# Optimization experiments

Hardware: AMD Instinct MI355X
Metric: run time of the kernel (lower is better)

Reference implementation:

```python
import jax, jax.numpy as jnp
import numpy as np

TEMPERATURE = 100.0  # exponential-smoothing temperature from __init__ default
ETA = 1.0            # feature/label cost tradeoff


def _cdist(a, b):
    # Euclidean distance matrix [M, N] between rows of a [M, D] and b [N, D]
    sq = (jnp.sum(a * a, axis=1)[:, None]
          + jnp.sum(b * b, axis=1)[None, :]
          - 2.0 * (a @ b.T))
    return jnp.sqrt(jnp.maximum(sq, 1e-12))


def setup_inputs() -> dict:
    key = jax.random.key(0)
    ks = jax.random.split(key, 9)
    B, Nt, Ns, H, Wd, C = 1024, 8192, 8192, 32, 32, 10
    D = H * Wd
    x = jax.random.normal(ks[0], (B, H, Wd), jnp.float32)
    target_features = jax.random.normal(ks[1], (Nt, H, Wd), jnp.float32)
    aligned_source_features = jax.random.normal(ks[2], (Nt, H, Wd), jnp.float32)
    source_features = jax.random.normal(ks[3], (Ns, H, Wd), jnp.float32)
    source_high_dim_labels = jax.random.uniform(ks[4], (Ns, C), jnp.float32)
    aligned_target_labels = jax.random.uniform(ks[5], (Ns, C), jnp.float32)
    source_label_distances = jax.random.uniform(ks[6], (C, C), jnp.float32)
    W = jax.random.normal(ks[7], (D, C), jnp.float32) * 0.02
    b = jnp.zeros((C,), jnp.float32)
    return {
        "x": x,
        "target_features": target_features,
        "aligned_source_features": aligned_source_features,
        "source_features": source_features,
        "source_high_dim_labels": source_high_dim_labels,
        "aligned_target_labels": aligned_target_labels,
        "source_label_distances": source_label_distances,
        "W": W,
        "b": b,
    }


def reference(x, target_features, aligned_source_features, source_features,
              source_high_dim_labels, aligned_target_labels,
              source_label_distances, W, b):
    B = x.shape[0]
    xf = x.reshape(B, -1)                                   # [B, D]
    tf = target_features.reshape(target_features.shape[0], -1)       # [Nt, D]
    asf = aligned_source_features.reshape(aligned_source_features.shape[0], -1)  # [Nt, D]
    sf = source_features.reshape(source_features.shape[0], -1)       # [Ns, D]

    # --- feature transport: target -> source (plain_softmax) ---
    d_feat = _cdist(xf, tf)                                 # [B, Nt]
    w_feat = jax.nn.softmax(-TEMPERATURE * d_feat, axis=1)  # [B, Nt]
    x_src = w_feat @ asf                                    # [B, D] in source space

    # --- source model (linear classifier head -> soft predictions) ---
    preds = jax.nn.softmax(x_src @ W + b, axis=1)           # [B, C]

    # --- label transport: source -> target (plain_softmax) ---
    cost = _cdist(x_src, sf)                                # feature_dists=True: [B, Ns]
    # label_dists=True: cost of moving predicted label mass to each sample's label
    cost = cost + ETA * (preds @ source_label_distances @ source_high_dim_labels.T)
    w_lab = jax.nn.softmax(-TEMPERATURE * cost, axis=1)     # [B, Ns]
    y = w_lab @ aligned_target_labels                       # [B, C] in target label space
    return y
```

## Files before the change

### kernel.cpp

```cpp
#include <hip/hip_runtime.h>
#include <hip/hip_bf16.h>
#include <math.h>

#define B_ROWS 1024
#define NT 8192
#define NS 8192
#define DIM 1024
#define NC 10
#define TEMP 100.0f
#define WCAP 1024
#define PREP_RPB 8

typedef __bf16 bf16x8 __attribute__((ext_vector_type(8)));
typedef __bf16 bf16x4 __attribute__((ext_vector_type(4)));
typedef float f32x4 __attribute__((ext_vector_type(4)));

#define GLOAD_LDS(g, l) \
    __builtin_amdgcn_global_load_lds((__attribute__((address_space(1))) void*)(g), \
                                     (__attribute__((address_space(3))) void*)(l), 16, 0, 0)

__device__ inline __bf16 split_hi(float v) { return (__bf16)v; }
__device__ inline __bf16 split_lo(float v) {
    __bf16 h = (__bf16)v;
    return (__bf16)(v - (float)h);
}

__device__ inline float wave_max(float v) {
    #pragma unroll
    for (int off = 32; off > 0; off >>= 1)
        v = fmaxf(v, __shfl_down(v, off, 64));
    return v;
}
__device__ inline float wave_sum(float v) {
    #pragma unroll
    for (int off = 32; off > 0; off >>= 1)
        v += __shfl_down(v, off, 64);
    return v;
}

__global__ __launch_bounds__(256) void k_prep0(const float* __restrict__ x,
                                               const float* __restrict__ tf,
                                               const float* __restrict__ sf,
                                               const float* __restrict__ sld,
                                               const float* __restrict__ shdl,
                                               const float* __restrict__ atl,
                                               __bf16* __restrict__ x2,
                                               __bf16* __restrict__ tf2,
                                               __bf16* __restrict__ sf2,
                                               float* __restrict__ nx_,
                                               float* __restrict__ nt_,
                                               float* __restrict__ ns_,
                                               float* __restrict__ M2Tt,
                                               float* __restrict__ atlt) {
    __shared__ float sred[4][PREP_RPB];
    __shared__ float sldL[NC * NC];
    const int NXB = B_ROWS / PREP_RPB;
    const int NTB = NT / PREP_RPB;
    const int NSB = NS / PREP_RPB;
    int b = blockIdx.x;
    int tid = threadIdx.x;
    if (b < NXB + NTB + NSB) {
        const float* Xp; __bf16* X2p; float* np; int r0;
        if (b < NXB)            { Xp = x;  X2p = x2;  np = nx_; r0 = b * PREP_RPB; }
        else if (b < NXB + NTB) { Xp = tf; X2p = tf2; np = nt_; r0 = (b - NXB) * PREP_RPB; }
        else                    { Xp = sf; X2p = sf2; np = ns_; r0 = (b - NXB - NTB) * PREP_RPB; }
        int c = tid * 4;
        int lane = tid & 63, wid = tid >> 6;
        #pragma unroll
        for (int r = 0; r < PREP_RPB; r++) {
            float4 v = *(const float4*)(Xp + (size_t)(r0 + r) * DIM + c);
            bf16x4 h, l;
            h[0] = split_hi(v.x); l[0] = split_lo(v.x);
            h[1] = split_hi(v.y); l[1] = split_lo(v.y);
            h[2] = split_hi(v.z); l[2] = split_lo(v.z);
            h[3] = split_hi(v.w); l[3] = split_lo(v.w);
            *(bf16x4*)(X2p + (size_t)(r0 + r) * 2048 + c) = h;
            *(bf16x4*)(X2p + (size_t)(r0 + r) * 2048 + 1024 + c) = l;
            float acc = v.x * v.x + v.y * v.y + v.z * v.z + v.w * v.w;
            float w = wave_sum(acc);
            if (lane == 0) sred[wid][r] = w;
        }
        __syncthreads();
        if (tid < PREP_RPB)
            np[r0 + tid] = sred[0][tid] + sred[1][tid] + sred[2][tid] + sred[3][tid];
    } else {
        if (tid < NC * NC) sldL[tid] = sld[tid];
        __syncthreads();
        int j = (b - NXB - NTB - NSB) * 256 + tid;
        float sh[NC], at[NC];
        #pragma unroll
        for (int k = 0; k < NC; k++) sh[k] = shdl[(size_t)j * NC + k];
        #pragma unroll
        for (int c = 0; c < NC; c++) at[c] = atl[(size_t)j * NC + c];
        #pragma unroll
        for (int c = 0; c < NC; c++) {
            float t = 0.f;
            #pragma unroll
            for (int k = 0; k < NC; k++) t += sldL[c * NC + k] * sh[k];
            M2Tt[c * NS + j] = t;
            atlt[c * NS + j] = at[c];
        }
    }
}

template <bool LOGITS>
__global__ __launch_bounds__(256) void k_gemm3(const __bf16* __restrict__ A2,
                                               const __bf16* __restrict__ B2,
                                               float* __restrict__ C,
                                               int M, int N, int K, int ksplit,
                                               const float* __restrict__ rowN,
                                               const float* __restrict__ colN) {
    __shared__ unsigned short AhS[8192], AlS[8192], BhS[8192], BlS[8192];
    __shared__ float extraL[LOGITS ? 256 : 2];
    float* rnL = extraL;
    float* cnL = extraL + 128;

    int tid = threadIdx.x;
    int wid = tid >> 6, lane = tid & 63;
    int wm = (wid >> 1) * 64, wn = (wid & 1) * 64;
    int id = blockIdx.y * gridDim.x + blockIdx.x;
    int bn_i = ((id >> 6) << 3) | (id & 7);
    int bm_i = (id >> 3) & 7;
    int bm = bm_i * 128, bn = bn_i * 128;
    size_t K2 = 2 * (size_t)K;
    int k_begin = blockIdx.z * ksplit;
    int nsteps = ksplit >> 6;

    if (LOGITS) {
        if (tid < 128) rnL[tid] = rowN[bm + tid];
        else cnL[tid - 128] = colN[bn + tid - 128];
    }

    f32x4 acc[4][4];
    #pragma unroll
    for (int i = 0; i < 4; i++)
        #pragma unroll
        for (int j = 0; j < 4; j++) acc[i][j] = (f32x4){0.f, 0.f, 0.f, 0.f};

    int r_in = lane >> 3;
    int cgo = ((lane & 7) ^ r_in) * 8;
    const __bf16* gA = A2 + (size_t)(bm + wid * 32 + r_in) * K2 + k_begin + cgo;
    const __bf16* gB = B2 + (size_t)(bn + wid * 32 + r_in) * K2 + k_begin + cgo;
    char* AhB = (char*)AhS; char* AlB = (char*)AlS;
    char* BhB = (char*)BhS; char* BlB = (char*)BlS;
    int lbw = wid * 4096;
    size_t row8 = 8 * K2;

    int ra = lane & 15, q = lane >> 4;
    int aoff[4][2], boff[4][2];
    #pragma unroll
    for (int i = 0; i < 4; i++) {
        #pragma unroll
        for (int kh = 0; kh < 2; kh++) {
            int chunk = ((kh << 2) | q) ^ (ra & 7);
            aoff[i][kh] = (wm + i * 16 + ra) * 64 + chunk * 8;
            boff[i][kh] = (wn + i * 16 + ra) * 64 + chunk * 8;
        }
    }
    const __bf16* AhE = (const __bf16*)AhS;
    const __bf16* AlE = (const __bf16*)AlS;
    const __bf16* BhE = (const __bf16*)BhS;
    const __bf16* BlE = (const __bf16*)BlS;

    for (int ks = 0; ks < nsteps; ks++) {
        __syncthreads();
        #pragma unroll
        for (int p = 0; p < 4; p++) {
            size_t go = p * row8;
            int lo = lbw + p * 1024;
            GLOAD_LDS(gA + go, AhB + lo);
            GLOAD_LDS(gA + go + K, AlB + lo);
            GLOAD_LDS(gB + go, BhB + lo);
            GLOAD_LDS(gB + go + K, BlB + lo);
        }
        gA += 64; gB += 64;
        __syncthreads();

        #pragma unroll
        for (int kh = 0; kh < 2; kh++) {
            bf16x8 ah[4], al[4];
            #pragma unroll
            for (int mi = 0; mi < 4; mi++) {
                ah[mi] = *(const bf16x8*)(AhE + aoff[mi][kh]);
                al[mi] = *(const bf16x8*)(AlE + aoff[mi][kh]);
            }
            #pragma unroll
            for (int ni = 0; ni < 4; ni++) {
                bf16x8 bh = *(const bf16x8*)(BhE + boff[ni][kh]);
                bf16x8 bl = *(const bf16x8*)(BlE + boff[ni][kh]);
                #pragma unroll
                for (int mi = 0; mi < 4; mi++) {
                    acc[mi][ni] = __builtin_amdgcn_mfma_f32_16x16x32_bf16(ah[mi], bh, acc[mi][ni], 0, 0, 0);
                    acc[mi][ni] = __builtin_amdgcn_mfma_f32_16x16x32_bf16(ah[mi], bl, acc[mi][ni], 0, 0, 0);
                    acc[mi][ni] = __builtin_amdgcn_mfma_f32_16x16x32_bf16(al[mi], bh, acc[mi][ni], 0, 0, 0);
                }
            }
        }
    }

    if (!LOGITS) {
        float* Cb = C + (size_t)blockIdx.z * M * N;
        #pragma unroll
        for (int mi = 0; mi < 4; mi++) {
            #pragma unroll
            for (int ni = 0; ni < 4; ni++) {
                int r0 = bm + wm + mi * 16 + q * 4;
                int c0 = bn + wn + ni * 16 + ra;
                Cb[(size_t)(r0 + 0) * N + c0] = acc[mi][ni][0];
                Cb[(size_t)(r0 + 1) * N + c0] = acc[mi][ni][1];
                Cb[(size_t)(r0 + 2) * N + c0] = acc[mi][ni][2];
                Cb[(size_t)(r0 + 3) * N + c0] = acc[mi][ni][3];
            }
        }
    } else {
        #pragma unroll
        for (int mi = 0; mi < 4; mi++) {
            #pragma unroll
            for (int ni = 0; ni < 4; ni++) {
                int cl = wn + ni * 16 + ra;
                float cn = cnL[cl];
                #pragma unroll
                for (int i = 0; i < 4; i++) {
                    int rl = wm + mi * 16 + q * 4 + i;
                    float sq = rnL[rl] + cn - 2.f * acc[mi][ni][i];
                    float d = sqrtf(fmaxf(sq, 1e-12f));
                    C[(size_t)(bm + rl) * N + bn + cl] = -TEMP * d;
                }
            }
        }
    }
}

__global__ __launch_bounds__(256) void k_xsrc(const float* __restrict__ S,
                                              const float* __restrict__ asf,
                                              const float* __restrict__ W,
                                              const float* __restrict__ bias,
                                              __bf16* __restrict__ xsrc2,
                                              float* __restrict__ nx2_,
                                              float* __restrict__ preds) {
    __shared__ float sm[4];
    __shared__ float ss[4];
    __shared__ int   sidx[WCAP];
    __shared__ float swt[WCAP];
    __shared__ int   scnt;
    __shared__ float red[4][NC + 1];
    int row = blockIdx.x;
    int tid = threadIdx.x;
    int lane = tid & 63, wid = tid >> 6;
    if (tid == 0) scnt = 0;
    const float4* sr = (const float4*)(S + (size_t)row * NT);
    float4 vals[NT / 1024];
    float lmax = -1e30f;
    #pragma unroll
    for (int u = 0; u < NT / 1024; u++) {
        float4 v = sr[tid + u * 256];
        vals[u] = v;
        lmax = fmaxf(fmaxf(fmaxf(v.x, v.y), fmaxf(v.z, v.w)), lmax);
    }
    float wmx = wave_max(lmax);
    if (lane == 0) sm[wid] = wmx;
    __syncthreads();
    float bmax = fmaxf(fmaxf(sm[0], sm[1]), fmaxf(sm[2], sm[3]));
    float lsum = 0.f;
    #pragma unroll
    for (int u = 0; u < NT / 1024; u++) {
        float4 v = vals[u];
        v.x = __expf(v.x - bmax); v.y = __expf(v.y - bmax);
        v.z = __expf(v.z - bmax); v.w = __expf(v.w - bmax);
        vals[u] = v;
        lsum += v.x + v.y + v.z + v.w;
    }
    float wsv = wave_sum(lsum);
    if (lane == 0) ss[wid] = wsv;
    __syncthreads();
    float bsum = ss[0] + ss[1] + ss[2] + ss[3];
    float inv = 1.0f / bsum;
    float thr = 1e-8f * bsum;
    #pragma unroll
    for (int u = 0; u < NT / 1024; u++) {
        float4 v = vals[u];
        int j = (tid + u * 256) * 4;
        if (v.x > thr) { int k = atomicAdd(&scnt, 1); if (k < WCAP) { sidx[k] = j;     swt[k] = v.x * inv; } }
        if (v.y > thr) { int k = atomicAdd(&scnt, 1); if (k < WCAP) { sidx[k] = j + 1; swt[k] = v.y * inv; } }
        if (v.z > thr) { int k = atomicAdd(&scnt, 1); if (k < WCAP) { sidx[k] = j + 2; swt[k] = v.z * inv; } }
        if (v.w > thr) { int k = atomicAdd(&scnt, 1); if (k < WCAP) { sidx[k] = j + 3; swt[k] = v.w * inv; } }
    }
    __syncthreads();
    int cnt = scnt < WCAP ? scnt : WCAP;
    int c = tid * 4;
    float sx = 0.f, sy = 0.f, sz = 0.f, sw = 0.f;
    for (int i = 0; i < cnt; i++) {
        float wg = swt[i];
        float4 v = *(const float4*)(asf + (size_t)sidx[i] * DIM + c);
        sx += wg * v.x; sy += wg * v.y; sz += wg * v.z; sw += wg * v.w;
    }
    bf16x4 h, l;
    h[0] = split_hi(sx); l[0] = split_lo(sx);
    h[1] = split_hi(sy); l[1] = split_lo(sy);
    h[2] = split_hi(sz); l[2] = split_lo(sz);
    h[3] = split_hi(sw); l[3] = split_lo(sw);
    *(bf16x4*)(xsrc2 + (size_t)row * 2048 + c) = h;
    *(bf16x4*)(xsrc2 + (size_t)row * 2048 + 1024 + c) = l;
    float accn = sx * sx + sy * sy + sz * sz + sw * sw;
    float accp[NC];
    #pragma unroll
    for (int cc = 0; cc < NC; cc++)
        accp[cc] = sx * W[(c + 0) * NC + cc] + sy * W[(c + 1) * NC + cc]
                 + sz * W[(c + 2) * NC + cc] + sw * W[(c + 3) * NC + cc];
    accn = wave_sum(accn);
    #pragma unroll
    for (int cc = 0; cc < NC; cc++) accp[cc] = wave_sum(accp[cc]);
    if (lane == 0) {
        red[wid][0] = accn;
        #pragma unroll
        for (int cc = 0; cc < NC; cc++) red[wid][1 + cc] = accp[cc];
    }
    __syncthreads();
    if (tid == 0) {
        nx2_[row] = red[0][0] + red[1][0] + red[2][0] + red[3][0];
        float lo[NC];
        float m = -1e30f;
        #pragma unroll
        for (int cc = 0; cc < NC; cc++) {
            lo[cc] = red[0][1 + cc] + red[1][1 + cc] + red[2][1 + cc] + red[3][1 + cc]
                   + bias[cc];
            m = fmaxf(m, lo[cc]);
        }
        float ssum = 0.f;
        #pragma unroll
        for (int cc = 0; cc < NC; cc++) {
            lo[cc] = __expf(lo[cc] - m);
            ssum += lo[cc];
        }
        float iv = 1.0f / ssum;
        #pragma unroll
        for (int cc = 0; cc < NC; cc++) preds[(size_t)row * NC + cc] = lo[cc] * iv;
    }
}

__global__ __launch_bounds__(256) void k_lab_softmax_y(const float* __restrict__ S,
                                                       const float* __restrict__ predsG,
                                                       const float* __restrict__ M2Tt,
                                                       const float* __restrict__ atlt,
                                                       float* __restrict__ y) {
    int r0 = blockIdx.x * 2, r1 = r0 + 1;
    float pr0[NC], pr1[NC];
    #pragma unroll
    for (int c = 0; c < NC; c++) {
        pr0[c] = TEMP * predsG[(size_t)r0 * NC + c];
        pr1[c] = TEMP * predsG[(size_t)r1 * NC + c];
    }
    const float4* s0 = (const float4*)(S + (size_t)r0 * NS);
    const float4* s1 = (const float4*)(S + (size_t)r1 * NS);
    const float4* M2 = (const float4*)M2Tt;
    const float4* AT = (const float4*)atlt;
    float4 v0[NS / 1024], v1[NS / 1024];
    float m0 = -1e30f, m1 = -1e30f;
    #pragma unroll
    for (int u = 0; u < NS / 1024; u++) {
        int j4 = threadIdx.x + u * 256;
        float4 a = s0[j4], b = s1[j4];
        float4 lab0 = make_float4(0.f, 0.f, 0.f, 0.f);
        float4 lab1 = make_float4(0.f, 0.f, 0.f, 0.f);
        #pragma unroll
        for (int c = 0; c < NC; c++) {
            float4 mv = M2[c * 2048 + j4];
            lab0.x += pr0[c] * mv.x; lab0.y += pr0[c] * mv.y;
            lab0.z += pr0[c] * mv.z; lab0.w += pr0[c] * mv.w;
            lab1.x += pr1[c] * mv.x; lab1.y += pr1[c] * mv.y;
            lab1.z += pr1[c] * mv.z; lab1.w += pr1[c] * mv.w;
        }
        a.x -= lab0.x; a.y -= lab0.y;
        a.z -= lab0.z; a.w -= lab0.w;
        b.x -= lab1.x; b.y -= lab1.y;
        b.z -= lab1.z; b.w -= lab1.w;
        v0[u] = a; v1[u] = b;
        m0 = fmaxf(m0, fmaxf(fmaxf(a.x, a.y), fmaxf(a.z, a.w)));
        m1 = fmaxf(m1, fmaxf(fmaxf(b.x, b.y), fmaxf(b.z, b.w)));
    }
    __shared__ float sm[2][4];
    __shared__ float ss[2][4];
    __shared__ float yred[4][2][NC];
    int lane = threadIdx.x & 63, wid = threadIdx.x >> 6;
    float wm0 = wave_max(m0), wm1 = wave_max(m1);
    if (lane == 0) { sm[0][wid] = wm0; sm[1][wid] = wm1; }
    __syncthreads();
    float bm0 = fmaxf(fmaxf(sm[0][0], sm[0][1]), fmaxf(sm[0][2], sm[0][3]));
    float bm1 = fmaxf(fmaxf(sm[1][0], sm[1][1]), fmaxf(sm[1][2], sm[1][3]));
    float ls0 = 0.f, ls1 = 0.f;
    #pragma unroll
    for (int u = 0; u < NS / 1024; u++) {
        float4 a = v0[u], b = v1[u];
        a.x = __expf(a.x - bm0); a.y = __expf(a.y - bm0);
        a.z = __expf(a.z - bm0); a.w = __expf(a.w - bm0);
        b.x = __expf(b.x - bm1); b.y = __expf(b.y - bm1);
        b.z = __expf(b.z - bm1); b.w = __expf(b.w - bm1);
        v0[u] = a; v1[u] = b;
        ls0 += a.x + a.y + a.z + a.w;
        ls1 += b.x + b.y + b.z + b.w;
    }
    float ws0 = wave_sum(ls0), ws1 = wave_sum(ls1);
    if (lane == 0) { ss[0][wid] = ws0; ss[1][wid] = ws1; }
    __syncthreads();
    float inv0 = 1.0f / (ss[0][0] + ss[0][1] + ss[0][2] + ss[0][3]);
    float inv1 = 1.0f / (ss[1][0] + ss[1][1] + ss[1][2] + ss[1][3]);
    float y0[NC] = {}, y1[NC] = {};
    #pragma unroll
    for (int u = 0; u < NS / 1024; u++) {
        int j4 = threadIdx.x + u * 256;
        float4 a = v0[u], b = v1[u];
        #pragma unroll
        for (int c = 0; c < NC; c++) {
            float4 av = AT[c * 2048 + j4];
            y0[c] += a.x * av.x + a.y * av.y + a.z * av.z + a.w * av.w;
            y1[c] += b.x * av.x + b.y * av.y + b.z * av.z + b.w * av.w;
        }
    }
    #pragma unroll
    for (int c = 0; c < NC; c++) {
        y0[c] = wave_sum(y0[c]) * inv0;
        y1[c] = wave_sum(y1[c]) * inv1;
    }
    if (lane == 0) {
        #pragma unroll
        for (int c = 0; c < NC; c++) { yred[wid][0][c] = y0[c]; yred[wid][1][c] = y1[c]; }
    }
    __syncthreads();
    if (threadIdx.x < 2 * NC) {
        int r = threadIdx.x / NC, c = threadIdx.x - r * NC;
        y[(size_t)(r0 + r) * NC + c] = yred[0][r][c] + yred[1][r][c] + yred[2][r][c] + yred[3][r][c];
    }
}

extern "C" void kernel_launch(void* const* d_in, const int* in_sizes, int n_in,
                              void* d_out, int out_size, void* d_ws, size_t ws_size,
                              hipStream_t stream) {
    const float* x    = (const float*)d_in[0];
    const float* tf   = (const float*)d_in[1];
    const float* asf  = (const float*)d_in[2];
    const float* sf   = (const float*)d_in[3];
    const float* shdl = (const float*)d_in[4];
    const float* atl  = (const float*)d_in[5];
    const float* sld  = (const float*)d_in[6];
    const float* W    = (const float*)d_in[7];
    const float* bias = (const float*)d_in[8];
    float* y = (float*)d_out;

    char* wsb = (char*)d_ws;
    float*  S     = (float*)(wsb);
    __bf16* tf2   = (__bf16*)(wsb + (32u << 20));
    __bf16* sf2   = (__bf16*)(wsb + (64u << 20));
    __bf16* x2    = (__bf16*)(wsb + (96u << 20));
    __bf16* xsrc2 = (__bf16*)(wsb + (100u << 20));
    float*  nt_   = (float*)(wsb + (108u << 20));
    float*  ns_   = nt_ + NT;
    float*  nx_   = ns_ + NS;
    float*  nx2_  = nx_ + B_ROWS;
    float*  preds = nx2_ + B_ROWS;
    float*  M2Tt  = preds + B_ROWS * NC;
    float*  atlt  = M2Tt + NS * NC;

    {
        int nblk = B_ROWS / PREP_RPB + NT / PREP_RPB + NS / PREP_RPB + NS / 256;
        k_prep0<<<nblk, 256, 0, stream>>>(x, tf, sf, sld, shdl, atl,
                                          x2, tf2, sf2, nx_, nt_, ns_, M2Tt, atlt);
    }

    {
        dim3 g(NT / 128, B_ROWS / 128, 1);
        k_gemm3<true><<<g, 256, 0, stream>>>(x2, tf2, S, B_ROWS, NT, DIM, DIM,
                                             nx_, nt_);
    }

    k_xsrc<<<B_ROWS, 256, 0, stream>>>(S, asf, W, bias, xsrc2, nx2_, preds);

    {
        dim3 g(NS / 128, B_ROWS / 128, 1);
        k_gemm3<true><<<g, 256, 0, stream>>>(xsrc2, sf2, S, B_ROWS, NS, DIM, DIM,
                                             nx2_, ns_);
    }
    k_lab_softmax_y<<<B_ROWS / 2, 256, 0, stream>>>(S, preds, M2Tt, atlt, y);
}
```

Before: 269.6 us.

## Double-buffer LDS tiles in split-bf16 GEMM with per-wave array loading

```diff
diff --git a/kernel.cpp b/kernel.cpp
--- a/kernel.cpp
+++ b/kernel.cpp
@@ -110,7 +110,8 @@
                                                int M, int N, int K, int ksplit,
                                                const float* __restrict__ rowN,
                                                const float* __restrict__ colN) {
-    __shared__ unsigned short AhS[8192], AlS[8192], BhS[8192], BlS[8192];
+    __shared__ __align__(16) unsigned short AhS[2][4096], AlS[2][4096];
+    __shared__ __align__(16) unsigned short BhS[2][4096], BlS[2][4096];
     __shared__ float extraL[LOGITS ? 256 : 2];
     float* rnL = extraL;
     float* cnL = extraL + 128;
@@ -124,7 +125,7 @@
     int bm = bm_i * 128, bn = bn_i * 128;
     size_t K2 = 2 * (size_t)K;
     int k_begin = blockIdx.z * ksplit;
-    int nsteps = ksplit >> 6;
+    int nsteps = ksplit >> 5;
 
     if (LOGITS) {
         if (tid < 128) rnL[tid] = rowN[bm + tid];
@@ -137,66 +138,66 @@
         #pragma unroll
         for (int j = 0; j < 4; j++) acc[i][j] = (f32x4){0.f, 0.f, 0.f, 0.f};
 
-    int r_in = lane >> 3;
-    int cgo = ((lane & 7) ^ r_in) * 8;
-    const __bf16* gA = A2 + (size_t)(bm + wid * 32 + r_in) * K2 + k_begin + cgo;
-    const __bf16* gB = B2 + (size_t)(bn + wid * 32 + r_in) * K2 + k_begin + cgo;
-    char* AhB = (char*)AhS; char* AlB = (char*)AlS;
-    char* BhB = (char*)BhS; char* BlB = (char*)BlS;
-    int lbw = wid * 4096;
-    size_t row8 = 8 * K2;
+    char* arrB = (wid == 0) ? (char*)AhS : (wid == 1) ? (char*)AlS
+               : (wid == 2) ? (char*)BhS : (char*)BlS;
+    const __bf16* gbase = (wid < 2) ? A2 : B2;
+    int rbase = (wid < 2) ? bm : bn;
+    int hilo = (wid & 1) ? K : 0;
+    int srow = lane >> 2;
+    int kperm = 8 * ((lane & 3) ^ ((lane >> 3) & 3));
+    const __bf16* gw = gbase + (size_t)(rbase + srow) * K2 + hilo + k_begin + kperm;
+    size_t row16 = 16 * K2;
 
     int ra = lane & 15, q = lane >> 4;
-    int aoff[4][2], boff[4][2];
+    int slot = q ^ ((ra >> 1) & 3);
+    int aoff[4], boff[4];
     #pragma unroll
     for (int i = 0; i < 4; i++) {
-        #pragma unroll
-        for (int kh = 0; kh < 2; kh++) {
-            int chunk = ((kh << 2) | q) ^ (ra & 7);
-            aoff[i][kh] = (wm + i * 16 + ra) * 64 + chunk * 8;
-            boff[i][kh] = (wn + i * 16 + ra) * 64 + chunk * 8;
-        }
-    }
-    const __bf16* AhE = (const __bf16*)AhS;
-    const __bf16* AlE = (const __bf16*)AlS;
-    const __bf16* BhE = (const __bf16*)BhS;
-    const __bf16* BlE = (const __bf16*)BlS;
-
+        aoff[i] = (wm + i * 16 + ra) * 32 + slot * 8;
+        boff[i] = (wn + i * 16 + ra) * 32 + slot * 8;
+    }
+
+#define STAGE(buf, koff) do {                                                  \
+        const __bf16* _g = gw + (koff);                                        \
+        char* _d = arrB + (buf) * 8192;                                        \
+        _Pragma("unroll")                                                      \
+        for (int p = 0; p < 8; p++)                                            \
+            GLOAD_LDS(_g + (size_t)p * row16, _d + p * 1024);                  \
+    } while (0)
+
+    STAGE(0, 0);
+    __syncthreads();
+
+    int cur = 0;
     for (int ks = 0; ks < nsteps; ks++) {
-        __syncthreads();
-        #pragma unroll
-        for (int p = 0; p < 4; p++) {
-            size_t go = p * row8;
-            int lo = lbw + p * 1024;
-            GLOAD_LDS(gA + go, AhB + lo);
-            GLOAD_LDS(gA + go + K, AlB + lo);
-            GLOAD_LDS(gB + go, BhB + lo);
-            GLOAD_LDS(gB + go + K, BlB + lo);
-        }
-        gA += 64; gB += 64;
-        __syncthreads();
-
-        #pragma unroll
-        for (int kh = 0; kh < 2; kh++) {
-            bf16x8 ah[4], al[4];
+        if (ks + 1 < nsteps) STAGE(cur ^ 1, (ks + 1) * 32);
+
+        const __bf16* AhE = (const __bf16*)&AhS[cur][0];
+        const __bf16* AlE = (const __bf16*)&AlS[cur][0];
+        const __bf16* BhE = (const __bf16*)&BhS[cur][0];
+        const __bf16* BlE = (const __bf16*)&BlS[cur][0];
+
+        bf16x8 ah[4], al[4];
+        #pragma unroll
+        for (int mi = 0; mi < 4; mi++) {
+            ah[mi] = *(const bf16x8*)(AhE + aoff[mi]);
+            al[mi] = *(const bf16x8*)(AlE + aoff[mi]);
+        }
+        #pragma unroll
+        for (int ni = 0; ni < 4; ni++) {
+            bf16x8 bh = *(const bf16x8*)(BhE + boff[ni]);
+            bf16x8 bl = *(const bf16x8*)(BlE + boff[ni]);
             #pragma unroll
             for (int mi = 0; mi < 4; mi++) {
-                ah[mi] = *(const bf16x8*)(AhE + aoff[mi][kh]);
-                al[mi] = *(const bf16x8*)(AlE + aoff[mi][kh]);
+                acc[mi][ni] = __builtin_amdgcn_mfma_f32_16x16x32_bf16(ah[mi], bh, acc[mi][ni], 0, 0, 0);
+                acc[mi][ni] = __builtin_amdgcn_mfma_f32_16x16x32_bf16(ah[mi], bl, acc[mi][ni], 0, 0, 0);
+                acc[mi][ni] = __builtin_amdgcn_mfma_f32_16x16x32_bf16(al[mi], bh, acc[mi][ni], 0, 0, 0);
             }
-            #pragma unroll
-            for (int ni = 0; ni < 4; ni++) {
-                bf16x8 bh = *(const bf16x8*)(BhE + boff[ni][kh]);
-                bf16x8 bl = *(const bf16x8*)(BlE + boff[ni][kh]);
-                #pragma unroll
-                for (int mi = 0; mi < 4; mi++) {
-                    acc[mi][ni] = __builtin_amdgcn_mfma_f32_16x16x32_bf16(ah[mi], bh, acc[mi][ni], 0, 0, 0);
-                    acc[mi][ni] = __builtin_amdgcn_mfma_f32_16x16x32_bf16(ah[mi], bl, acc[mi][ni], 0, 0, 0);
-                    acc[mi][ni] = __builtin_amdgcn_mfma_f32_16x16x32_bf16(al[mi], bh, acc[mi][ni], 0, 0, 0);
-                }
-            }
-        }
-    }
+        }
+        __syncthreads();
+        cur ^= 1;
+    }
+#undef STAGE
 
     if (!LOGITS) {
         float* Cb = C + (size_t)blockIdx.z * M * N;
```

Result: slower. 279.3 us (+3.6%).

## Use 512-thread blocks in split-bf16 distance GEMM with per-wave array loading

Applied to the files above, without the earlier changes.

```diff
diff --git a/kernel.cpp b/kernel.cpp
--- a/kernel.cpp
+++ b/kernel.cpp
@@ -104,12 +104,12 @@
 }
 
 template <bool LOGITS>
-__global__ __launch_bounds__(256) void k_gemm3(const __bf16* __restrict__ A2,
-                                               const __bf16* __restrict__ B2,
-                                               float* __restrict__ C,
-                                               int M, int N, int K, int ksplit,
-                                               const float* __restrict__ rowN,
-                                               const float* __restrict__ colN) {
+__global__ __launch_bounds__(512, 4) void k_gemm3(const __bf16* __restrict__ A2,
+                                                  const __bf16* __restrict__ B2,
+                                                  float* __restrict__ C,
+                                                  int M, int N, int K, int ksplit,
+                                                  const float* __restrict__ rowN,
+                                                  const float* __restrict__ colN) {
     __shared__ unsigned short AhS[8192], AlS[8192], BhS[8192], BlS[8192];
     __shared__ float extraL[LOGITS ? 256 : 2];
     float* rnL = extraL;
@@ -117,7 +117,7 @@
 
     int tid = threadIdx.x;
     int wid = tid >> 6, lane = tid & 63;
-    int wm = (wid >> 1) * 64, wn = (wid & 1) * 64;
+    int wm = (wid >> 2) * 64, wn = (wid & 3) * 32;
     int id = blockIdx.y * gridDim.x + blockIdx.x;
     int bn_i = ((id >> 6) << 3) | (id & 7);
     int bm_i = (id >> 3) & 7;
@@ -128,33 +128,40 @@
 
     if (LOGITS) {
         if (tid < 128) rnL[tid] = rowN[bm + tid];
-        else cnL[tid - 128] = colN[bn + tid - 128];
-    }
-
-    f32x4 acc[4][4];
+        else if (tid < 256) cnL[tid - 128] = colN[bn + tid - 128];
+    }
+
+    f32x4 acc[4][2];
     #pragma unroll
     for (int i = 0; i < 4; i++)
         #pragma unroll
-        for (int j = 0; j < 4; j++) acc[i][j] = (f32x4){0.f, 0.f, 0.f, 0.f};
-
+        for (int j = 0; j < 2; j++) acc[i][j] = (f32x4){0.f, 0.f, 0.f, 0.f};
+
+    int arr = wid & 3, hh = wid >> 2;
+    char* arrB = (arr == 0) ? (char*)AhS : (arr == 1) ? (char*)AlS
+               : (arr == 2) ? (char*)BhS : (char*)BlS;
+    const __bf16* gbase = (arr < 2) ? A2 : B2;
+    int rbase = (arr < 2) ? bm : bn;
+    int hilo = (arr & 1) ? K : 0;
     int r_in = lane >> 3;
     int cgo = ((lane & 7) ^ r_in) * 8;
-    const __bf16* gA = A2 + (size_t)(bm + wid * 32 + r_in) * K2 + k_begin + cgo;
-    const __bf16* gB = B2 + (size_t)(bn + wid * 32 + r_in) * K2 + k_begin + cgo;
-    char* AhB = (char*)AhS; char* AlB = (char*)AlS;
-    char* BhB = (char*)BhS; char* BlB = (char*)BlS;
-    int lbw = wid * 4096;
+    const __bf16* gw = gbase + (size_t)(rbase + hh * 64 + r_in) * K2 + hilo + k_begin + cgo;
+    int ldst = hh * 8192;
     size_t row8 = 8 * K2;
 
     int ra = lane & 15, q = lane >> 4;
-    int aoff[4][2], boff[4][2];
-    #pragma unroll
-    for (int i = 0; i < 4; i++) {
-        #pragma unroll
-        for (int kh = 0; kh < 2; kh++) {
+    int aoff[4][2], boff[2][2];
+    #pragma unroll
+    for (int kh = 0; kh < 2; kh++) {
+        #pragma unroll
+        for (int i = 0; i < 4; i++) {
             int chunk = ((kh << 2) | q) ^ (ra & 7);
             aoff[i][kh] = (wm + i * 16 + ra) * 64 + chunk * 8;
-            boff[i][kh] = (wn + i * 16 + ra) * 64 + chunk * 8;
+        }
+        #pragma unroll
+        for (int j = 0; j < 2; j++) {
+            int chunk = ((kh << 2) | q) ^ (ra & 7);
+            boff[j][kh] = (wn + j * 16 + ra) * 64 + chunk * 8;
         }
     }
     const __bf16* AhE = (const __bf16*)AhS;
@@ -165,15 +172,10 @@
     for (int ks = 0; ks < nsteps; ks++) {
         __syncthreads();
         #pragma unroll
-        for (int p = 0; p < 4; p++) {
-            size_t go = p * row8;
-            int lo = lbw + p * 1024;
-            GLOAD_LDS(gA + go, AhB + lo);
-            GLOAD_LDS(gA + go + K, AlB + lo);
-            GLOAD_LDS(gB + go, BhB + lo);
-            GLOAD_LDS(gB + go + K, BlB + lo);
-        }
-        gA += 64; gB += 64;
+        for (int p = 0; p < 8; p++) {
+            GLOAD_LDS(gw + (size_t)p * row8, arrB + ldst + p * 1024);
+        }
+        gw += 64;
         __syncthreads();
 
         #pragma unroll
@@ -185,7 +187,7 @@
                 al[mi] = *(const bf16x8*)(AlE + aoff[mi][kh]);
             }
             #pragma unroll
-            for (int ni = 0; ni < 4; ni++) {
+            for (int ni = 0; ni < 2; ni++) {
                 bf16x8 bh = *(const bf16x8*)(BhE + boff[ni][kh]);
                 bf16x8 bl = *(const bf16x8*)(BlE + boff[ni][kh]);
                 #pragma unroll
@@ -203,7 +205,7 @@
         #pragma unroll
         for (int mi = 0; mi < 4; mi++) {
             #pragma unroll
-            for (int ni = 0; ni < 4; ni++) {
+            for (int ni = 0; ni < 2; ni++) {
                 int r0 = bm + wm + mi * 16 + q * 4;
                 int c0 = bn + wn + ni * 16 + ra;
                 Cb[(size_t)(r0 + 0) * N + c0] = acc[mi][ni][0];
@@ -216,7 +218,7 @@
         #pragma unroll
         for (int mi = 0; mi < 4; mi++) {
             #pragma unroll
-            for (int ni = 0; ni < 4; ni++) {
+            for (int ni = 0; ni < 2; ni++) {
                 int cl = wn + ni * 16 + ra;
                 float cn = cnL[cl];
                 #pragma unroll
@@ -468,7 +470,7 @@
 
     {
         dim3 g(NT / 128, B_ROWS / 128, 1);
-        k_gemm3<true><<<g, 256, 0, stream>>>(x2, tf2, S, B_ROWS, NT, DIM, DIM,
+        k_gemm3<true><<<g, 512, 0, stream>>>(x2, tf2, S, B_ROWS, NT, DIM, DIM,
                                              nx_, nt_);
     }
 
@@ -476,7 +478,7 @@
 
     {
         dim3 g(NS / 128, B_ROWS / 128, 1);
-        k_gemm3<true><<<g, 256, 0, stream>>>(xsrc2, sf2, S, B_ROWS, NS, DIM, DIM,
+        k_gemm3<true><<<g, 512, 0, stream>>>(xsrc2, sf2, S, B_ROWS, NS, DIM, DIM,
                                              nx2_, ns_);
     }
     k_lab_softmax_y<<<B_ROWS / 2, 256, 0, stream>>>(S, preds, M2Tt, atlt, y);
```

After: 272.1 us. About the same (+0.9%).
